# Performance work log

Measured on AMD Instinct MI355X. Metric: run time of the kernel, lower is better.

## Reference

```python
import jax, jax.numpy as jnp
import numpy as np

N = 50000      # num_nodes
E = 800000     # num_edges (before self loops)
EMB = 128      # emb_dim
GH = 64        # gcn_hidden
TD = 4         # temporal_dim
B = 64         # batch of sequences
T = 200        # max sequence length
H = 128        # lstm_hidden (per direction)
IN_DIM = 2 + EMB + TD


def lstm_scan(x_tbi, w_ih, w_hh, b_ih, b_hh):
    """x_tbi: [T, B, I] -> hidden states [T, B, H]. PyTorch gate order i,f,g,o."""
    Bsz = x_tbi.shape[1]
    Hh = w_hh.shape[1]

    def step(carry, xt):
        h, c = carry
        g = xt @ w_ih.T + h @ w_hh.T + b_ih + b_hh
        i, f, gg, o = jnp.split(g, 4, axis=-1)
        c = jax.nn.sigmoid(f) * c + jax.nn.sigmoid(i) * jnp.tanh(gg)
        h = jax.nn.sigmoid(o) * jnp.tanh(c)
        return (h, c), h

    init = (jnp.zeros((Bsz, Hh), x_tbi.dtype), jnp.zeros((Bsz, Hh), x_tbi.dtype))
    _, hs = jax.lax.scan(step, init, x_tbi)
    return hs


def gcn_layer(x, W, b, src, dst, ew):
    """PyG GCNConv: linear -> symmetric-norm gather/scatter-add -> bias.
    (self loops already appended to src/dst/ew by caller)"""
    h = x @ W  # [N, out]
    deg = jax.ops.segment_sum(ew, dst, num_segments=N)
    dinv = jnp.where(deg > 0, jax.lax.rsqrt(deg), 0.0)
    norm = dinv[src] * ew * dinv[dst]            # [E+N]
    msg = h[src] * norm[:, None]                  # gather + scale
    return jax.ops.segment_sum(msg, dst, num_segments=N) + b


def setup_inputs() -> dict:
    key = jax.random.key(0)
    ks = jax.random.split(key, 16)
    s = 0.02
    return {
        'x_coords': jax.random.normal(ks[0], (N, 2), jnp.float32),
        'temporal_features': jax.random.uniform(ks[1], (N, TD), jnp.float32, -1.0, 1.0),
        'edge_index': jax.random.randint(ks[2], (2, E), 0, N),
        'edge_weight': jnp.ones((E,), jnp.float32),
        'seq': jax.random.randint(ks[3], (B, T), 0, N),
        'lengths': jax.random.randint(ks[4], (B,), 1, T + 1),
        'node_emb': jax.random.normal(ks[5], (N, EMB), jnp.float32) * s,
        'gcn1_w': jax.random.normal(ks[6], (IN_DIM, GH), jnp.float32) * s,
        'gcn1_b': jnp.zeros((GH,), jnp.float32),
        'gcn2_w': jax.random.normal(ks[7], (GH, EMB), jnp.float32) * s,
        'gcn2_b': jnp.zeros((EMB,), jnp.float32),
        'w_ih_f': jax.random.normal(ks[8], (4 * H, EMB), jnp.float32) * s,
        'w_hh_f': jax.random.normal(ks[9], (4 * H, H), jnp.float32) * s,
        'b_ih_f': jnp.zeros((4 * H,), jnp.float32),
        'b_hh_f': jnp.zeros((4 * H,), jnp.float32),
        'w_ih_b': jax.random.normal(ks[10], (4 * H, EMB), jnp.float32) * s,
        'w_hh_b': jax.random.normal(ks[11], (4 * H, H), jnp.float32) * s,
        'b_ih_b': jnp.zeros((4 * H,), jnp.float32),
        'b_hh_b': jnp.zeros((4 * H,), jnp.float32),
        'attn_w': jax.random.normal(ks[12], (2 * H,), jnp.float32) * s,
        'attn_b': jnp.zeros((), jnp.float32),
        'fc_w': jax.random.normal(ks[13], (2 * H, N), jnp.float32) * s,
        'fc_b': jnp.zeros((N,), jnp.float32),
    }


def reference(x_coords, temporal_features, edge_index, edge_weight, seq, lengths,
              node_emb, gcn1_w, gcn1_b, gcn2_w, gcn2_b,
              w_ih_f, w_hh_f, b_ih_f, b_hh_f,
              w_ih_b, w_hh_b, b_ih_b, b_hh_b,
              attn_w, attn_b, fc_w, fc_b):
    # --- GCN with self loops (PyG add_self_loops=True, fill_value=1) ---
    loop = jnp.arange(N)
    src = jnp.concatenate([edge_index[0], loop])
    dst = jnp.concatenate([edge_index[1], loop])
    ew = jnp.concatenate([edge_weight, jnp.ones((N,), edge_weight.dtype)])

    x = jnp.concatenate([x_coords, node_emb, temporal_features], axis=1)  # [N, 134]
    z = jax.nn.relu(gcn_layer(x, gcn1_w, gcn1_b, src, dst, ew))
    z = gcn_layer(z, gcn2_w, gcn2_b, src, dst, ew)  # dropout = identity (eval)

    # --- sequence embedding + BiLSTM ---
    seq_emb = z[seq]                                  # [B, T, EMB]
    h_f = lstm_scan(seq_emb.transpose(1, 0, 2), w_ih_f, w_hh_f, b_ih_f, b_hh_f)
    h_f = h_f.transpose(1, 0, 2)                      # [B, T, H]

    # backward direction: reverse each sequence within its valid length
    t = jnp.arange(T)
    valid = t[None, :] < lengths[:, None]             # [B, T]
    rev_idx = jnp.where(valid, lengths[:, None] - 1 - t[None, :], t[None, :])
    x_rev = jnp.take_along_axis(seq_emb, rev_idx[:, :, None], axis=1)
    h_b = lstm_scan(x_rev.transpose(1, 0, 2), w_ih_b, w_hh_b, b_ih_b, b_hh_b)
    h_b = jnp.take_along_axis(h_b.transpose(1, 0, 2), rev_idx[:, :, None], axis=1)

    lstm_out = jnp.concatenate([h_f, h_b], axis=-1)   # [B, T, 2H]

    # --- masked attention pooling ---
    scores = lstm_out @ attn_w + attn_b               # [B, T]
    scores = jnp.where(valid, scores, -jnp.inf)
    aw = jax.nn.softmax(scores, axis=1)
    context = jnp.einsum('bt,btd->bd', aw, lstm_out)  # [B, 2H]

    return context @ fc_w + fc_b                      # [B, N]
```

## Files before the change

### kernel.cpp

```cpp
#include <hip/hip_runtime.h>
#include <math.h>

#define NN 50000
#define NE 800000
#define EMB 128
#define GH 64
#define BB 64
#define TT 200
#define HH 128
#define G4 512
#define IND 134
#define PM 128
#define PO 128

__device__ __forceinline__ float sigf(float x) { return 1.0f / (1.0f + __expf(-x)); }
__device__ __forceinline__ float tanhf_(float x) { return 1.0f - 2.0f / (__expf(2.0f * x) + 1.0f); }
__device__ __forceinline__ void fma4(float4& a, float s, const float4 w) {
    a.x += s * w.x; a.y += s * w.y; a.z += s * w.z; a.w += s * w.w;
}

__global__ void hist_kernel(const int* __restrict__ ei, const float* __restrict__ ew,
                            int* __restrict__ cnt, float* __restrict__ degw) {
    int e = blockIdx.x * 256 + threadIdx.x;
    if (e >= NE) return;
    int d = ei[NE + e];
    atomicAdd(&cnt[d], 1);
    atomicAdd(&degw[d], ew[e]);
}

__global__ void dinv_kernel(const float* __restrict__ degw, float* __restrict__ dinv) {
    int n = blockIdx.x * 256 + threadIdx.x;
    if (n >= NN) return;
    dinv[n] = rsqrtf(degw[n] + 1.0f);
}

__global__ __launch_bounds__(1024) void scan1_kernel(const int* __restrict__ cnt,
                                                     int* __restrict__ rs, int* __restrict__ partials) {
    __shared__ int s[1024];
    int gid = blockIdx.x * 1024 + threadIdx.x;
    int v = (gid < NN) ? cnt[gid] : 0;
    s[threadIdx.x] = v;
    __syncthreads();
    for (int off = 1; off < 1024; off <<= 1) {
        int add = (threadIdx.x >= (unsigned)off) ? s[threadIdx.x - off] : 0;
        __syncthreads();
        s[threadIdx.x] += add;
        __syncthreads();
    }
    if (gid < NN) rs[gid] = s[threadIdx.x] - v;
    if (threadIdx.x == 1023) partials[blockIdx.x] = s[1023];
}

__global__ void scan2_kernel(int* __restrict__ partials, int nblk) {
    if (threadIdx.x == 0) {
        int acc = 0;
        for (int i = 0; i < nblk; ++i) { int v = partials[i]; partials[i] = acc; acc += v; }
    }
}

__global__ __launch_bounds__(1024) void scan3_kernel(const int* __restrict__ partials,
                                                     int* __restrict__ rs, int* __restrict__ cursor) {
    int gid = blockIdx.x * 1024 + threadIdx.x;
    if (gid < NN) {
        int v = rs[gid] + partials[gid >> 10];
        rs[gid] = v;
        cursor[gid] = v;
    }
    if (gid == 0) rs[NN] = NE;
}

__global__ void fill_kernel(const int* __restrict__ ei, const float* __restrict__ ew,
                            const float* __restrict__ dinv, int* __restrict__ cursor,
                            int* __restrict__ ssrc, float* __restrict__ sw) {
    int e = blockIdx.x * 256 + threadIdx.x;
    if (e >= NE) return;
    int s = ei[e], d = ei[NE + e];
    int pos = atomicAdd(&cursor[d], 1);
    ssrc[pos] = s;
    sw[pos] = ew[e] * dinv[s] * dinv[d];
}

__global__ __launch_bounds__(256) void gemm1_kernel(const float* __restrict__ coords,
                                                    const float* __restrict__ temporal,
                                                    const float* __restrict__ emb,
                                                    const float* __restrict__ W1,
                                                    float* __restrict__ h1) {
    __shared__ __align__(16) float wl[IND][GH];
    for (int i = threadIdx.x; i < IND * GH / 4; i += 256)
        ((float4*)wl)[i] = ((const float4*)W1)[i];
    __syncthreads();
    int n = blockIdx.x * 256 + threadIdx.x;
    if (n >= NN) return;
    float4 acc[16];
    float c0 = coords[2 * n], c1 = coords[2 * n + 1];
#pragma unroll
    for (int j = 0; j < 16; ++j) {
        float4 wa = *(const float4*)&wl[0][j * 4];
        float4 wb = *(const float4*)&wl[1][j * 4];
        float4 a;
        a.x = c0 * wa.x + c1 * wb.x; a.y = c0 * wa.y + c1 * wb.y;
        a.z = c0 * wa.z + c1 * wb.z; a.w = c0 * wa.w + c1 * wb.w;
        acc[j] = a;
    }
    const float4* er = (const float4*)(emb + (size_t)n * EMB);
#pragma unroll 2
    for (int k4 = 0; k4 < 32; ++k4) {
        float4 v = er[k4];
        int k = 2 + k4 * 4;
#pragma unroll
        for (int j = 0; j < 16; ++j) {
            fma4(acc[j], v.x, *(const float4*)&wl[k][j * 4]);
            fma4(acc[j], v.y, *(const float4*)&wl[k + 1][j * 4]);
            fma4(acc[j], v.z, *(const float4*)&wl[k + 2][j * 4]);
            fma4(acc[j], v.w, *(const float4*)&wl[k + 3][j * 4]);
        }
    }
    float t0 = temporal[4 * n], t1 = temporal[4 * n + 1], t2 = temporal[4 * n + 2], t3 = temporal[4 * n + 3];
#pragma unroll
    for (int j = 0; j < 16; ++j) {
        fma4(acc[j], t0, *(const float4*)&wl[130][j * 4]);
        fma4(acc[j], t1, *(const float4*)&wl[131][j * 4]);
        fma4(acc[j], t2, *(const float4*)&wl[132][j * 4]);
        fma4(acc[j], t3, *(const float4*)&wl[133][j * 4]);
        *(float4*)&h1[(size_t)n * GH + j * 4] = acc[j];
    }
}

__global__ __launch_bounds__(256) void agg_kernel(const float* __restrict__ hin,
                                                  const int* __restrict__ rs,
                                                  const int* __restrict__ ssrc,
                                                  const float* __restrict__ sw,
                                                  const float* __restrict__ dinv,
                                                  const float* __restrict__ bias, int relu,
                                                  float* __restrict__ hout) {
    int lane = threadIdx.x & 63;
    int wid = threadIdx.x >> 6;
    int n = blockIdx.x * 4 + wid;
    if (n >= NN) return;
    float dv = dinv[n];
    float acc = hin[(size_t)n * GH + lane] * (dv * dv);
    int i = rs[n], e1 = rs[n + 1];
    for (; i + 3 < e1; i += 4) {
        int s0 = ssrc[i], s1 = ssrc[i + 1], s2 = ssrc[i + 2], s3 = ssrc[i + 3];
        float w0 = sw[i], w1 = sw[i + 1], w2 = sw[i + 2], w3 = sw[i + 3];
        float a0 = hin[(size_t)s0 * GH + lane];
        float a1 = hin[(size_t)s1 * GH + lane];
        float a2 = hin[(size_t)s2 * GH + lane];
        float a3 = hin[(size_t)s3 * GH + lane];
        acc += a0 * w0 + a1 * w1 + a2 * w2 + a3 * w3;
    }
    for (; i < e1; ++i) acc += hin[(size_t)ssrc[i] * GH + lane] * sw[i];
    if (bias) acc += bias[lane];
    if (relu) acc = fmaxf(acc, 0.0f);
    hout[(size_t)n * GH + lane] = acc;
}

__global__ void w2t_kernel(const float* __restrict__ W2, float* __restrict__ w2t) {
    int i = blockIdx.x * 256 + threadIdx.x;
    if (i >= GH * EMB) return;
    int o = i >> 6, k = i & 63;
    w2t[i] = W2[(size_t)k * EMB + o];
}

__global__ __launch_bounds__(256) void gemm2_kernel(const float* __restrict__ a2,
                                                    const float* __restrict__ w2t,
                                                    const float* __restrict__ b2,
                                                    float* __restrict__ z2) {
    int m0 = blockIdx.x * 128, o0 = blockIdx.y * 64;
    __shared__ __align__(16) float xs[128][64];
    __shared__ __align__(16) float wt[64][64];
    __shared__ float bsh[64];
    int tid = threadIdx.x;
#pragma unroll
    for (int i = 0; i < 8; ++i) {
        int idx = i * 256 + tid;
        int r = idx >> 4, c4 = idx & 15;
        int m = m0 + r;
        float4 v = (m < NN) ? *(const float4*)&a2[(size_t)m * GH + c4 * 4]
                            : make_float4(0.f, 0.f, 0.f, 0.f);
        *(float4*)&xs[r][(c4 ^ ((r >> 2) & 3)) * 4] = v;
    }
#pragma unroll
    for (int i = 0; i < 4; ++i) {
        int idx = i * 256 + tid;
        int r = idx >> 4, c4 = idx & 15;
        float4 v = *(const float4*)&w2t[(size_t)(o0 + r) * GH + c4 * 4];
        *(float4*)&wt[r][(c4 ^ ((r >> 3) & 7)) * 4] = v;
    }
    if (tid < 64) bsh[tid] = b2[o0 + tid];
    __syncthreads();
    int mt = tid >> 3, ot = tid & 7;
    float acc[4][8];
#pragma unroll
    for (int mi = 0; mi < 4; ++mi)
#pragma unroll
        for (int oi = 0; oi < 8; ++oi) acc[mi][oi] = 0.0f;
    for (int k4 = 0; k4 < 16; ++k4) {
        int xc = (k4 ^ (mt & 3)) * 4;
        int wc = (k4 ^ (ot & 7)) * 4;
        float4 xv[4], wv[8];
#pragma unroll
        for (int mi = 0; mi < 4; ++mi) xv[mi] = *(const float4*)&xs[mt * 4 + mi][xc];
#pragma unroll
        for (int oi = 0; oi < 8; ++oi) wv[oi] = *(const float4*)&wt[ot * 8 + oi][wc];
#pragma unroll
        for (int mi = 0; mi < 4; ++mi)
#pragma unroll
            for (int oi = 0; oi < 8; ++oi)
                acc[mi][oi] += xv[mi].x * wv[oi].x + xv[mi].y * wv[oi].y
                             + xv[mi].z * wv[oi].z + xv[mi].w * wv[oi].w;
    }
#pragma unroll
    for (int mi = 0; mi < 4; ++mi) {
        int m = m0 + mt * 4 + mi;
        if (m >= NN) continue;
        int ob = ot * 8;
        float4 oa = make_float4(acc[mi][0] + bsh[ob + 0], acc[mi][1] + bsh[ob + 1],
                                acc[mi][2] + bsh[ob + 2], acc[mi][3] + bsh[ob + 3]);
        float4 obv = make_float4(acc[mi][4] + bsh[ob + 4], acc[mi][5] + bsh[ob + 5],
                                 acc[mi][6] + bsh[ob + 6], acc[mi][7] + bsh[ob + 7]);
        *(float4*)&z2[(size_t)m * EMB + o0 + ob] = oa;
        *(float4*)&z2[(size_t)m * EMB + o0 + ob + 4] = obv;
    }
}

__global__ void gather_kernel(const int* __restrict__ seq, const float* __restrict__ z2,
                              float* __restrict__ se) {
    int idx = blockIdx.x * 256 + threadIdx.x;
    if (idx >= BB * TT * 32) return;
    int r = idx >> 5, q = idx & 31;
    int node = seq[r];
    ((float4*)se)[(size_t)r * 32 + q] = ((const float4*)z2)[(size_t)node * 32 + q];
}

__global__ __launch_bounds__(256) void pregemm_kernel(const float* __restrict__ se,
                                                      const float* __restrict__ w_ih_f,
                                                      const float* __restrict__ w_ih_b,
                                                      const float* __restrict__ b_ih_f,
                                                      const float* __restrict__ b_hh_f,
                                                      const float* __restrict__ b_ih_b,
                                                      const float* __restrict__ b_hh_b,
                                                      const int* __restrict__ lengths,
                                                      float* __restrict__ xpf,
                                                      float* __restrict__ xpb) {
    int dir = blockIdx.z;
    const float* w_ih = dir ? w_ih_b : w_ih_f;
    int o0 = blockIdx.y * PO;
    int m0 = blockIdx.x * PM;
    __shared__ __align__(16) float xs[PM][EMB];
    __shared__ __align__(16) float ws[PO][EMB];
    __shared__ float bsh[PO];
    int tid = threadIdx.x;
#pragma unroll
    for (int i = 0; i < 16; ++i) {
        int idx = i * 256 + tid;
        int row = idx >> 5, c4 = idx & 31;
        float4 v = *(const float4*)&w_ih[(size_t)(o0 + row) * EMB + c4 * 4];
        *(float4*)&ws[row][(c4 ^ ((row >> 3) & 7)) * 4] = v;
    }
    if (tid < PO) bsh[tid] = dir ? (b_ih_b[o0 + tid] + b_hh_b[o0 + tid])
                                 : (b_ih_f[o0 + tid] + b_hh_f[o0 + tid]);
#pragma unroll
    for (int i = 0; i < 16; ++i) {
        int idx = i * 256 + tid;
        int r = idx >> 5, c4 = idx & 31;
        int m = m0 + r;
        int t = m >> 6, b = m & 63;
        int tsrc = t;
        if (dir) { int len = lengths[b]; tsrc = (t < len) ? (len - 1 - t) : t; }
        float4 v = *(const float4*)&se[((size_t)b * TT + tsrc) * EMB + c4 * 4];
        *(float4*)&xs[r][(c4 ^ ((r >> 3) & 3)) * 4] = v;
    }
    __syncthreads();
    int mt = tid >> 4, ot = tid & 15;
    int mswz = mt & 3, oswz = ot & 7;
    float acc[8][8];
#pragma unroll
    for (int mi = 0; mi < 8; ++mi)
#pragma unroll
        for (int oi = 0; oi < 8; ++oi) acc[mi][oi] = 0.0f;
    for (int k4 = 0; k4 < 32; ++k4) {
        int xk = (k4 ^ mswz) * 4;
        int wk = (k4 ^ oswz) * 4;
        float4 xv[8], wv[8];
#pragma unroll
        for (int mi = 0; mi < 8; ++mi) xv[mi] = *(const float4*)&xs[mt * 8 + mi][xk];
#pragma unroll
        for (int oi = 0; oi < 8; ++oi) wv[oi] = *(const float4*)&ws[ot * 8 + oi][wk];
#pragma unroll
        for (int mi = 0; mi < 8; ++mi)
#pragma unroll
            for (int oi = 0; oi < 8; ++oi)
                acc[mi][oi] += xv[mi].x * wv[oi].x + xv[mi].y * wv[oi].y
                             + xv[mi].z * wv[oi].z + xv[mi].w * wv[oi].w;
    }
    float* xp = dir ? xpb : xpf;
#pragma unroll
    for (int mi = 0; mi < 8; ++mi) {
        int m = m0 + mt * 8 + mi;
        int ob = ot * 8;
        float4 oa = make_float4(acc[mi][0] + bsh[ob + 0], acc[mi][1] + bsh[ob + 1],
                                acc[mi][2] + bsh[ob + 2], acc[mi][3] + bsh[ob + 3]);
        float4 obv = make_float4(acc[mi][4] + bsh[ob + 4], acc[mi][5] + bsh[ob + 5],
                                 acc[mi][6] + bsh[ob + 6], acc[mi][7] + bsh[ob + 7]);
        *(float4*)&xp[(size_t)m * G4 + o0 + ob] = oa;
        *(float4*)&xp[(size_t)m * G4 + o0 + ob + 4] = obv;
    }
}

__global__ __launch_bounds__(1024, 4) void lstm_kernel(const float* __restrict__ xpf,
                                                       const float* __restrict__ xpb,
                                                       const float* __restrict__ w_hh_f,
                                                       const float* __restrict__ w_hh_b,
                                                       const int* __restrict__ lengths,
                                                       float* __restrict__ hfo,
                                                       float* __restrict__ hbo) {
    int chain = blockIdx.x;
    int dir = chain & 1, b = chain >> 1;
    const float* w_hh = dir ? w_hh_b : w_hh_f;
    const float* xp = dir ? xpb : xpf;
    float* ho = dir ? hbo : hfo;
    int tid = threadIdx.x;
    int wv = tid >> 6, lane = tid & 63;
    int uu = lane >> 3, kq = lane & 7;
    int u = wv * 8 + uu;
    int len = lengths[b];

    float4 W[4][4];
#pragma unroll
    for (int g = 0; g < 4; ++g)
#pragma unroll
        for (int j4 = 0; j4 < 4; ++j4)
            W[g][j4] = *(const float4*)&w_hh[(size_t)(g * HH + u) * HH + kq * 16 + j4 * 4];

    __shared__ __align__(16) float hl[2][8][20];
    if (tid < 320) ((float*)hl)[tid] = 0.0f;
    __syncthreads();

    bool act = (kq == 0);
    const float* xb = xp + (size_t)b * G4 + u;
    float cst = 0.0f;
    float x0 = 0.f, x1 = 0.f, x2 = 0.f, x3 = 0.f;
    if (act && len > 0) { x0 = xb[0]; x1 = xb[HH]; x2 = xb[2 * HH]; x3 = xb[3 * HH]; }
    for (int t = 0; t < len; ++t) {
        const float4* h4 = (const float4*)&hl[t & 1][kq][0];
        float a0 = 0.f, a1 = 0.f, a2 = 0.f, a3 = 0.f;
#pragma unroll
        for (int j4 = 0; j4 < 4; ++j4) {
            float4 hv = h4[j4];
            a0 += W[0][j4].x * hv.x + W[0][j4].y * hv.y + W[0][j4].z * hv.z + W[0][j4].w * hv.w;
            a1 += W[1][j4].x * hv.x + W[1][j4].y * hv.y + W[1][j4].z * hv.z + W[1][j4].w * hv.w;
            a2 += W[2][j4].x * hv.x + W[2][j4].y * hv.y + W[2][j4].z * hv.z + W[2][j4].w * hv.w;
            a3 += W[3][j4].x * hv.x + W[3][j4].y * hv.y + W[3][j4].z * hv.z + W[3][j4].w * hv.w;
        }
#pragma unroll
        for (int m = 1; m < 8; m <<= 1) {
            a0 += __shfl_xor(a0, m, 64);
            a1 += __shfl_xor(a1, m, 64);
            a2 += __shfl_xor(a2, m, 64);
            a3 += __shfl_xor(a3, m, 64);
        }
        if (act) {
            float n0 = 0.f, n1 = 0.f, n2 = 0.f, n3 = 0.f;
            if (t + 1 < len) {
                const float* xn = xb + (size_t)(t + 1) * (BB * G4);
                n0 = xn[0]; n1 = xn[HH]; n2 = xn[2 * HH]; n3 = xn[3 * HH];
            }
            float gi = sigf(a0 + x0), gf = sigf(a1 + x1);
            float gg = tanhf_(a2 + x2), go = sigf(a3 + x3);
            cst = gf * cst + gi * gg;
            float h = go * tanhf_(cst);
            hl[(t + 1) & 1][u >> 4][u & 15] = h;
            int tt = dir ? (len - 1 - t) : t;
            ho[((size_t)b * TT + tt) * HH + u] = h;
            x0 = n0; x1 = n1; x2 = n2; x3 = n3;
        }
        __syncthreads();
    }
}

__global__ __launch_bounds__(256) void attn_kernel(const float* __restrict__ hf,
                                                   const float* __restrict__ hb,
                                                   const float* __restrict__ attn_w,
                                                   const float* __restrict__ attn_b,
                                                   const int* __restrict__ lengths,
                                                   float* __restrict__ ctx) {
    int b = blockIdx.x;
    int tid = threadIdx.x;
    int len = lengths[b];
    __shared__ __align__(16) float wl[256];
    __shared__ float pl[256];
    __shared__ float red[256];
    wl[tid] = attn_w[tid];
    __syncthreads();
    float sc = -3.0e38f;
    if (tid < len) {
        const float4* rf = (const float4*)(hf + ((size_t)b * TT + tid) * HH);
        const float4* rb = (const float4*)(hb + ((size_t)b * TT + tid) * HH);
        const float4* w4 = (const float4*)wl;
        float s = attn_b[0];
        for (int k4 = 0; k4 < 32; ++k4) {
            float4 a = rf[k4], ww = w4[k4];
            s += a.x * ww.x + a.y * ww.y + a.z * ww.z + a.w * ww.w;
        }
        for (int k4 = 0; k4 < 32; ++k4) {
            float4 a = rb[k4], ww = w4[32 + k4];
            s += a.x * ww.x + a.y * ww.y + a.z * ww.z + a.w * ww.w;
        }
        sc = s;
    }
    red[tid] = sc;
    __syncthreads();
    for (int off = 128; off > 0; off >>= 1) {
        if (tid < off) red[tid] = fmaxf(red[tid], red[tid + off]);
        __syncthreads();
    }
    float mx = red[0];
    __syncthreads();
    float e = (tid < len) ? __expf(sc - mx) : 0.0f;
    red[tid] = e;
    __syncthreads();
    for (int off = 128; off > 0; off >>= 1) {
        if (tid < off) red[tid] += red[tid + off];
        __syncthreads();
    }
    float inv = 1.0f / red[0];
    pl[tid] = e * inv;
    __syncthreads();
    float acc = 0.0f;
    const float* basep = (tid < HH) ? (hf + (size_t)b * TT * HH + tid)
                                    : (hb + (size_t)b * TT * HH + (tid - HH));
#pragma unroll 4
    for (int t = 0; t < len; ++t) acc += pl[t] * basep[(size_t)t * HH];
    ctx[(size_t)b * 256 + tid] = acc;
}

__global__ __launch_bounds__(256) void fc_kernel(const float* __restrict__ ctx,
                                                 const float* __restrict__ fc_w,
                                                 const float* __restrict__ fc_b,
                                                 float* __restrict__ out) {
    __shared__ __align__(16) float cl[64][256];
    for (int i = threadIdx.x; i < 64 * 256 / 4; i += 256)
        ((float4*)cl)[i] = ((const float4*)ctx)[i];
    __syncthreads();
    int nb = threadIdx.x & 63;
    int bq = threadIdx.x >> 6;
    int n = blockIdx.x * 64 + nb;
    if (n >= NN) return;
    float acc[16];
#pragma unroll
    for (int i = 0; i < 16; ++i) acc[i] = 0.0f;
#pragma unroll 2
    for (int k4 = 0; k4 < 64; ++k4) {
        int k = k4 * 4;
        float w0 = fc_w[(size_t)k * NN + n];
        float w1 = fc_w[(size_t)(k + 1) * NN + n];
        float w2 = fc_w[(size_t)(k + 2) * NN + n];
        float w3 = fc_w[(size_t)(k + 3) * NN + n];
#pragma unroll
        for (int i = 0; i < 16; ++i) {
            float4 cv = *(const float4*)&cl[bq * 16 + i][k];
            acc[i] += cv.x * w0 + cv.y * w1 + cv.z * w2 + cv.w * w3;
        }
    }
    float fb = fc_b[n];
#pragma unroll
    for (int i = 0; i < 16; ++i)
        out[(size_t)(bq * 16 + i) * NN + n] = acc[i] + fb;
}

extern "C" void kernel_launch(void* const* d_in, const int* in_sizes, int n_in,
                              void* d_out, int out_size, void* d_ws, size_t ws_size,
                              hipStream_t stream) {
    const float* x_coords   = (const float*)d_in[0];
    const float* temporal   = (const float*)d_in[1];
    const int*   edge_index = (const int*)d_in[2];
    const float* edge_w     = (const float*)d_in[3];
    const int*   seq        = (const int*)d_in[4];
    const int*   lengths    = (const int*)d_in[5];
    const float* node_emb   = (const float*)d_in[6];
    const float* gcn1_w     = (const float*)d_in[7];
    const float* gcn1_b     = (const float*)d_in[8];
    const float* gcn2_w     = (const float*)d_in[9];
    const float* gcn2_b     = (const float*)d_in[10];
    const float* w_ih_f     = (const float*)d_in[11];
    const float* w_hh_f     = (const float*)d_in[12];
    const float* b_ih_f     = (const float*)d_in[13];
    const float* b_hh_f     = (const float*)d_in[14];
    const float* w_ih_b     = (const float*)d_in[15];
    const float* w_hh_b     = (const float*)d_in[16];
    const float* b_ih_b     = (const float*)d_in[17];
    const float* b_hh_b     = (const float*)d_in[18];
    const float* attn_w     = (const float*)d_in[19];
    const float* attn_b     = (const float*)d_in[20];
    const float* fc_w       = (const float*)d_in[21];
    const float* fc_b       = (const float*)d_in[22];
    float* out = (float*)d_out;

    char* base = (char*)d_ws;
    size_t off = 0;
    auto alloc = [&](size_t nbytes) -> void* {
        void* p = base + off;
        off = (off + nbytes + 255) & ~(size_t)255;
        return p;
    };
    int*   cnt     = (int*)alloc((size_t)2 * NN * 4);
    float* degw    = (float*)(cnt + NN);
    float* dinv    = (float*)alloc((size_t)NN * 4);
    int*   rs      = (int*)alloc(((size_t)NN + 1) * 4);
    int*   cursor  = (int*)alloc((size_t)NN * 4);
    int*   partials= (int*)alloc(64 * 4);
    int*   ssrc    = (int*)alloc((size_t)NE * 4);
    float* sw      = (float*)alloc((size_t)NE * 4);
    float* h1      = (float*)alloc((size_t)NN * GH * 4);
    float* z1      = (float*)alloc((size_t)NN * GH * 4);
    float* a2      = h1;
    float* w2t     = (float*)alloc((size_t)GH * EMB * 4);
    float* z2      = (float*)alloc((size_t)NN * EMB * 4);
    float* se      = (float*)alloc((size_t)BB * TT * EMB * 4);
    float* xpf     = (float*)alloc((size_t)TT * BB * G4 * 4);
    float* xpb     = (float*)alloc((size_t)TT * BB * G4 * 4);
    float* hfo     = (float*)alloc((size_t)BB * TT * HH * 4);
    float* hbo     = (float*)alloc((size_t)BB * TT * HH * 4);
    float* ctx     = (float*)alloc((size_t)BB * 256 * 4);
    (void)ws_size; (void)in_sizes; (void)n_in; (void)out_size;

    hipMemsetAsync(cnt, 0, (size_t)2 * NN * 4, stream);

    hist_kernel<<<(NE + 255) / 256, 256, 0, stream>>>(edge_index, edge_w, cnt, degw);
    dinv_kernel<<<(NN + 255) / 256, 256, 0, stream>>>(degw, dinv);
    const int nblk = (NN + 1023) / 1024;
    scan1_kernel<<<nblk, 1024, 0, stream>>>(cnt, rs, partials);
    scan2_kernel<<<1, 64, 0, stream>>>(partials, nblk);
    scan3_kernel<<<nblk, 1024, 0, stream>>>(partials, rs, cursor);
    fill_kernel<<<(NE + 255) / 256, 256, 0, stream>>>(edge_index, edge_w, dinv, cursor, ssrc, sw);
    w2t_kernel<<<(GH * EMB + 255) / 256, 256, 0, stream>>>(gcn2_w, w2t);

    gemm1_kernel<<<(NN + 255) / 256, 256, 0, stream>>>(x_coords, temporal, node_emb, gcn1_w, h1);
    agg_kernel<<<(NN + 3) / 4, 256, 0, stream>>>(h1, rs, ssrc, sw, dinv, gcn1_b, 1, z1);
    agg_kernel<<<(NN + 3) / 4, 256, 0, stream>>>(z1, rs, ssrc, sw, dinv, (const float*)nullptr, 0, a2);
    gemm2_kernel<<<dim3((NN + 127) / 128, 2), 256, 0, stream>>>(a2, w2t, gcn2_b, z2);

    gather_kernel<<<(BB * TT * 32 + 255) / 256, 256, 0, stream>>>(seq, z2, se);
    pregemm_kernel<<<dim3(TT * BB / PM, G4 / PO, 2), 256, 0, stream>>>(
        se, w_ih_f, w_ih_b, b_ih_f, b_hh_f, b_ih_b, b_hh_b, lengths, xpf, xpb);
    lstm_kernel<<<BB * 2, 1024, 0, stream>>>(xpf, xpb, w_hh_f, w_hh_b, lengths, hfo, hbo);
    attn_kernel<<<BB, 256, 0, stream>>>(hfo, hbo, attn_w, attn_b, lengths, ctx);
    fc_kernel<<<(NN + 63) / 64, 256, 0, stream>>>(ctx, fc_w, fc_b, out);
}
```

Before: 701.0 us.

## Tile gemm1 in shared memory, reshape LSTM reduction, register-block fc

gemm1 now stages a 128-node input tile and a pre-transposed, reordered W1 in XOR-swizzled shared memory, and computes 4x8 register tiles per thread. A new w1t kernel produces that transposed W1. The LSTM kernel assigns one unit per thread across 8 k-slices and reduces partial sums through shared memory plus a block barrier, replacing the intra-wave shuffles and the double-buffered h. fc_kernel now has each thread handle 4 output columns, reusing each context load across them. The extra barrier per LSTM step and the higher shared-memory footprint may cost serial latency or occupancy.

```diff
diff --git a/kernel.cpp b/kernel.cpp
--- a/kernel.cpp
+++ b/kernel.cpp
@@ -80,49 +80,81 @@
     sw[pos] = ew[e] * dinv[s] * dinv[d];
 }
 
+__global__ void w1t_kernel(const float* __restrict__ W1, float* __restrict__ w1t) {
+    int i = blockIdx.x * 256 + threadIdx.x;
+    if (i >= 64 * 136) return;
+    int o = i / 136, j = i - (i / 136) * 136;
+    float v = 0.0f;
+    if (j < 128) v = W1[(size_t)(j + 2) * GH + o];
+    else if (j < 130) v = W1[(size_t)(j - 128) * GH + o];
+    else if (j < 134) v = W1[(size_t)j * GH + o];
+    w1t[i] = v;
+}
+
 __global__ __launch_bounds__(256) void gemm1_kernel(const float* __restrict__ coords,
                                                     const float* __restrict__ temporal,
                                                     const float* __restrict__ emb,
-                                                    const float* __restrict__ W1,
+                                                    const float* __restrict__ w1t,
                                                     float* __restrict__ h1) {
-    __shared__ __align__(16) float wl[IND][GH];
-    for (int i = threadIdx.x; i < IND * GH / 4; i += 256)
-        ((float4*)wl)[i] = ((const float4*)W1)[i];
-    __syncthreads();
-    int n = blockIdx.x * 256 + threadIdx.x;
-    if (n >= NN) return;
-    float4 acc[16];
-    float c0 = coords[2 * n], c1 = coords[2 * n + 1];
-#pragma unroll
-    for (int j = 0; j < 16; ++j) {
-        float4 wa = *(const float4*)&wl[0][j * 4];
-        float4 wb = *(const float4*)&wl[1][j * 4];
-        float4 a;
-        a.x = c0 * wa.x + c1 * wb.x; a.y = c0 * wa.y + c1 * wb.y;
-        a.z = c0 * wa.z + c1 * wb.z; a.w = c0 * wa.w + c1 * wb.w;
-        acc[j] = a;
-    }
-    const float4* er = (const float4*)(emb + (size_t)n * EMB);
-#pragma unroll 2
-    for (int k4 = 0; k4 < 32; ++k4) {
-        float4 v = er[k4];
-        int k = 2 + k4 * 4;
-#pragma unroll
-        for (int j = 0; j < 16; ++j) {
-            fma4(acc[j], v.x, *(const float4*)&wl[k][j * 4]);
-            fma4(acc[j], v.y, *(const float4*)&wl[k + 1][j * 4]);
-            fma4(acc[j], v.z, *(const float4*)&wl[k + 2][j * 4]);
-            fma4(acc[j], v.w, *(const float4*)&wl[k + 3][j * 4]);
+    __shared__ __align__(16) float xs[128][136];
+    __shared__ __align__(16) float wt[64][136];
+    int tid = threadIdx.x;
+    int m0 = blockIdx.x * 128;
+    for (int i = tid; i < 64 * 34; i += 256) {
+        int rr = i / 34, w = i - rr * 34;
+        float4 v = *(const float4*)&w1t[(size_t)rr * 136 + w * 4];
+        int ws = (w < 32) ? (w ^ ((rr >> 3) & 7)) : w;
+        *(float4*)&wt[rr][ws * 4] = v;
+    }
+    for (int i = tid; i < 128 * 32; i += 256) {
+        int r = i >> 5, c4 = i & 31;
+        int m = m0 + r;
+        float4 v = make_float4(0.f, 0.f, 0.f, 0.f);
+        if (m < NN) v = *(const float4*)&emb[(size_t)m * EMB + c4 * 4];
+        *(float4*)&xs[r][(c4 ^ ((r >> 2) & 7)) * 4] = v;
+    }
+    for (int i = tid; i < 128 * 8; i += 256) {
+        int r = i >> 3, c = i & 7;
+        int m = m0 + r;
+        float v = 0.0f;
+        if (m < NN) {
+            if (c < 2) v = coords[2 * m + c];
+            else if (c < 6) v = temporal[4 * m + (c - 2)];
         }
-    }
-    float t0 = temporal[4 * n], t1 = temporal[4 * n + 1], t2 = temporal[4 * n + 2], t3 = temporal[4 * n + 3];
-#pragma unroll
-    for (int j = 0; j < 16; ++j) {
-        fma4(acc[j], t0, *(const float4*)&wl[130][j * 4]);
-        fma4(acc[j], t1, *(const float4*)&wl[131][j * 4]);
-        fma4(acc[j], t2, *(const float4*)&wl[132][j * 4]);
-        fma4(acc[j], t3, *(const float4*)&wl[133][j * 4]);
-        *(float4*)&h1[(size_t)n * GH + j * 4] = acc[j];
+        xs[r][128 + c] = v;
+    }
+    __syncthreads();
+    int mt = tid >> 3, ot = tid & 7;
+    int xswz = mt & 7, wswz = ot & 7;
+    float acc[4][8];
+#pragma unroll
+    for (int mi = 0; mi < 4; ++mi)
+#pragma unroll
+        for (int oi = 0; oi < 8; ++oi) acc[mi][oi] = 0.0f;
+    for (int k4 = 0; k4 < 34; ++k4) {
+        int xk = (k4 < 32) ? (k4 ^ xswz) : k4;
+        int wk = (k4 < 32) ? (k4 ^ wswz) : k4;
+        float4 xv[4], wv[8];
+#pragma unroll
+        for (int mi = 0; mi < 4; ++mi) xv[mi] = *(const float4*)&xs[mt * 4 + mi][xk * 4];
+#pragma unroll
+        for (int oi = 0; oi < 8; ++oi) wv[oi] = *(const float4*)&wt[ot * 8 + oi][wk * 4];
+#pragma unroll
+        for (int mi = 0; mi < 4; ++mi)
+#pragma unroll
+            for (int oi = 0; oi < 8; ++oi)
+                acc[mi][oi] += xv[mi].x * wv[oi].x + xv[mi].y * wv[oi].y
+                             + xv[mi].z * wv[oi].z + xv[mi].w * wv[oi].w;
+    }
+#pragma unroll
+    for (int mi = 0; mi < 4; ++mi) {
+        int m = m0 + mt * 4 + mi;
+        if (m >= NN) continue;
+        int ob = ot * 8;
+        float4 oa = make_float4(acc[mi][0], acc[mi][1], acc[mi][2], acc[mi][3]);
+        float4 obv = make_float4(acc[mi][4], acc[mi][5], acc[mi][6], acc[mi][7]);
+        *(float4*)&h1[(size_t)m * GH + ob] = oa;
+        *(float4*)&h1[(size_t)m * GH + ob + 4] = obv;
     }
 }
 
@@ -321,9 +353,8 @@
     const float* xp = dir ? xpb : xpf;
     float* ho = dir ? hbo : hfo;
     int tid = threadIdx.x;
-    int wv = tid >> 6, lane = tid & 63;
-    int uu = lane >> 3, kq = lane & 7;
-    int u = wv * 8 + uu;
+    int u = tid & 127;
+    int kq = tid >> 7;
     int len = lengths[b];
 
     float4 W[4][4];
@@ -333,17 +364,19 @@
         for (int j4 = 0; j4 < 4; ++j4)
             W[g][j4] = *(const float4*)&w_hh[(size_t)(g * HH + u) * HH + kq * 16 + j4 * 4];
 
-    __shared__ __align__(16) float hl[2][8][20];
-    if (tid < 320) ((float*)hl)[tid] = 0.0f;
-    __syncthreads();
-
-    bool act = (kq == 0);
-    const float* xb = xp + (size_t)b * G4 + u;
+    __shared__ __align__(16) float hl[HH];
+    __shared__ __align__(16) float part[HH][9][4];
+    if (tid < HH) hl[tid] = 0.0f;
+    __syncthreads();
+
     float cst = 0.0f;
     float x0 = 0.f, x1 = 0.f, x2 = 0.f, x3 = 0.f;
-    if (act && len > 0) { x0 = xb[0]; x1 = xb[HH]; x2 = xb[2 * HH]; x3 = xb[3 * HH]; }
+    const float* xpt = xp + (size_t)b * G4 + u;
+    if (tid < HH && len > 0) {
+        x0 = xpt[0]; x1 = xpt[HH]; x2 = xpt[2 * HH]; x3 = xpt[3 * HH];
+    }
     for (int t = 0; t < len; ++t) {
-        const float4* h4 = (const float4*)&hl[t & 1][kq][0];
+        const float4* h4 = (const float4*)&hl[kq * 16];
         float a0 = 0.f, a1 = 0.f, a2 = 0.f, a3 = 0.f;
 #pragma unroll
         for (int j4 = 0; j4 < 4; ++j4) {
@@ -353,24 +386,24 @@
             a2 += W[2][j4].x * hv.x + W[2][j4].y * hv.y + W[2][j4].z * hv.z + W[2][j4].w * hv.w;
             a3 += W[3][j4].x * hv.x + W[3][j4].y * hv.y + W[3][j4].z * hv.z + W[3][j4].w * hv.w;
         }
-#pragma unroll
-        for (int m = 1; m < 8; m <<= 1) {
-            a0 += __shfl_xor(a0, m, 64);
-            a1 += __shfl_xor(a1, m, 64);
-            a2 += __shfl_xor(a2, m, 64);
-            a3 += __shfl_xor(a3, m, 64);
-        }
-        if (act) {
+        if (kq) *(float4*)&part[u][kq][0] = make_float4(a0, a1, a2, a3);
+        __syncthreads();
+        if (tid < HH) {
             float n0 = 0.f, n1 = 0.f, n2 = 0.f, n3 = 0.f;
             if (t + 1 < len) {
-                const float* xn = xb + (size_t)(t + 1) * (BB * G4);
+                const float* xn = xpt + (size_t)(t + 1) * (BB * G4);
                 n0 = xn[0]; n1 = xn[HH]; n2 = xn[2 * HH]; n3 = xn[3 * HH];
             }
-            float gi = sigf(a0 + x0), gf = sigf(a1 + x1);
-            float gg = tanhf_(a2 + x2), go = sigf(a3 + x3);
+            float s0 = x0 + a0, s1 = x1 + a1, s2 = x2 + a2, s3 = x3 + a3;
+#pragma unroll
+            for (int q = 1; q < 8; ++q) {
+                float4 p = *(const float4*)&part[u][q][0];
+                s0 += p.x; s1 += p.y; s2 += p.z; s3 += p.w;
+            }
+            float gi = sigf(s0), gf = sigf(s1), gg = tanhf_(s2), go = sigf(s3);
             cst = gf * cst + gi * gg;
             float h = go * tanhf_(cst);
-            hl[(t + 1) & 1][u >> 4][u & 15] = h;
+            hl[u] = h;
             int tt = dir ? (len - 1 - t) : t;
             ho[((size_t)b * TT + tt) * HH + u] = h;
             x0 = n0; x1 = n1; x2 = n2; x3 = n3;
@@ -443,30 +476,45 @@
     for (int i = threadIdx.x; i < 64 * 256 / 4; i += 256)
         ((float4*)cl)[i] = ((const float4*)ctx)[i];
     __syncthreads();
-    int nb = threadIdx.x & 63;
+    int lane = threadIdx.x & 63;
     int bq = threadIdx.x >> 6;
-    int n = blockIdx.x * 64 + nb;
-    if (n >= NN) return;
-    float acc[16];
-#pragma unroll
-    for (int i = 0; i < 16; ++i) acc[i] = 0.0f;
-#pragma unroll 2
+    int nb = blockIdx.x * 256 + lane;
+    float acc[16][4];
+#pragma unroll
+    for (int i = 0; i < 16; ++i)
+#pragma unroll
+        for (int c = 0; c < 4; ++c) acc[i][c] = 0.0f;
     for (int k4 = 0; k4 < 64; ++k4) {
         int k = k4 * 4;
-        float w0 = fc_w[(size_t)k * NN + n];
-        float w1 = fc_w[(size_t)(k + 1) * NN + n];
-        float w2 = fc_w[(size_t)(k + 2) * NN + n];
-        float w3 = fc_w[(size_t)(k + 3) * NN + n];
+        float w[4][4];
+#pragma unroll
+        for (int j = 0; j < 4; ++j)
+#pragma unroll
+            for (int c = 0; c < 4; ++c) {
+                int n = nb + c * 64;
+                w[j][c] = (n < NN) ? fc_w[(size_t)(k + j) * NN + n] : 0.0f;
+            }
 #pragma unroll
         for (int i = 0; i < 16; ++i) {
             float4 cv = *(const float4*)&cl[bq * 16 + i][k];
-            acc[i] += cv.x * w0 + cv.y * w1 + cv.z * w2 + cv.w * w3;
+#pragma unroll
+            for (int c = 0; c < 4; ++c)
+                acc[i][c] += cv.x * w[0][c] + cv.y * w[1][c] + cv.z * w[2][c] + cv.w * w[3][c];
         }
     }
-    float fb = fc_b[n];
+    float fb[4];
+#pragma unroll
+    for (int c = 0; c < 4; ++c) {
+        int n = nb + c * 64;
+        fb[c] = (n < NN) ? fc_b[n] : 0.0f;
+    }
 #pragma unroll
     for (int i = 0; i < 16; ++i)
-        out[(size_t)(bq * 16 + i) * NN + n] = acc[i] + fb;
+#pragma unroll
+        for (int c = 0; c < 4; ++c) {
+            int n = nb + c * 64;
+            if (n < NN) out[(size_t)(bq * 16 + i) * NN + n] = acc[i][c] + fb[c];
+        }
 }
 
 extern "C" void kernel_launch(void* const* d_in, const int* in_sizes, int n_in,
@@ -515,6 +563,7 @@
     float* h1      = (float*)alloc((size_t)NN * GH * 4);
     float* z1      = (float*)alloc((size_t)NN * GH * 4);
     float* a2      = h1;
+    float* w1t     = (float*)alloc((size_t)64 * 136 * 4);
     float* w2t     = (float*)alloc((size_t)GH * EMB * 4);
     float* z2      = (float*)alloc((size_t)NN * EMB * 4);
     float* se      = (float*)alloc((size_t)BB * TT * EMB * 4);
@@ -534,9 +583,10 @@
     scan2_kernel<<<1, 64, 0, stream>>>(partials, nblk);
     scan3_kernel<<<nblk, 1024, 0, stream>>>(partials, rs, cursor);
     fill_kernel<<<(NE + 255) / 256, 256, 0, stream>>>(edge_index, edge_w, dinv, cursor, ssrc, sw);
+    w1t_kernel<<<(64 * 136 + 255) / 256, 256, 0, stream>>>(gcn1_w, w1t);
     w2t_kernel<<<(GH * EMB + 255) / 256, 256, 0, stream>>>(gcn2_w, w2t);
 
-    gemm1_kernel<<<(NN + 255) / 256, 256, 0, stream>>>(x_coords, temporal, node_emb, gcn1_w, h1);
+    gemm1_kernel<<<(NN + 127) / 128, 256, 0, stream>>>(x_coords, temporal, node_emb, w1t, h1);
     agg_kernel<<<(NN + 3) / 4, 256, 0, stream>>>(h1, rs, ssrc, sw, dinv, gcn1_b, 1, z1);
     agg_kernel<<<(NN + 3) / 4, 256, 0, stream>>>(z1, rs, ssrc, sw, dinv, (const float*)nullptr, 0, a2);
     gemm2_kernel<<<dim3((NN + 127) / 128, 2), 256, 0, stream>>>(a2, w2t, gcn2_b, z2);
@@ -546,5 +596,5 @@
         se, w_ih_f, w_ih_b, b_ih_f, b_hh_f, b_ih_b, b_hh_b, lengths, xpf, xpb);
     lstm_kernel<<<BB * 2, 1024, 0, stream>>>(xpf, xpb, w_hh_f, w_hh_b, lengths, hfo, hbo);
     attn_kernel<<<BB, 256, 0, stream>>>(hfo, hbo, attn_w, attn_b, lengths, ctx);
-    fc_kernel<<<(NN + 63) / 64, 256, 0, stream>>>(ctx, fc_w, fc_b, out);
-}
+    fc_kernel<<<(NN + 255) / 256, 256, 0, stream>>>(ctx, fc_w, fc_b, out);
+}
```

After: 673.6 us. 1.04x faster.
